# Kernel optimization log

Hardware: AMD Instinct MI355X
Metric: run time of the kernel (lower is better)

Reference implementation:

```python
import jax, jax.numpy as jnp
import numpy as np

EPS = 1e-5
NH = 8   # num_heads
P = 8    # patch_size (local window)

def layernorm(x, g, b):
    m = jnp.mean(x, axis=-1, keepdims=True)
    v = jnp.var(x, axis=-1, keepdims=True)
    return (x - m) * jax.lax.rsqrt(v + EPS) * g + b

def axis_embed(pos, nf):
    # DETR-style interleaved sin/cos along one axis -> (L, nf)
    dim_t = 10000.0 ** (2.0 * (jnp.arange(nf) // 2).astype(jnp.float32) / nf)
    p = pos[:, None] / dim_t
    return jnp.stack([jnp.sin(p[:, 0::2]), jnp.cos(p[:, 1::2])], axis=-1).reshape(pos.shape[0], nf)

def pos_embed_2d(E, H, W):
    # (H, W, E): first half of channels encode y, second half encode x
    half = E // 2
    ye = axis_embed(jnp.arange(1, H + 1, dtype=jnp.float32), half)
    xe = axis_embed(jnp.arange(1, W + 1, dtype=jnp.float32), half)
    return jnp.concatenate([jnp.broadcast_to(ye[:, None, :], (H, W, half)),
                            jnp.broadcast_to(xe[None, :, :], (H, W, half))], axis=-1)

def pos_embed_1d(L, E):
    # standard sinusoidal, (L, 1, E)
    pos = jnp.arange(L, dtype=jnp.float32)[:, None]
    div = jnp.exp(jnp.arange(0, E, 2, dtype=jnp.float32) * (-np.log(10000.0) / E))
    pe = jnp.zeros((L, E), jnp.float32)
    pe = pe.at[:, 0::2].set(jnp.sin(pos * div)).at[:, 1::2].set(jnp.cos(pos * div))
    return pe[:, None, :]

def mha(q, k, v, Wq, bq, Wk, bk, Wv, bv, Wo, bo, nh):
    # q,k,v: (B, L, C)
    B, Lq, C = q.shape
    hd = C // nh
    qh = (q @ Wq + bq).reshape(B, Lq, nh, hd)
    kh = (k @ Wk + bk).reshape(B, -1, nh, hd)
    vh = (v @ Wv + bv).reshape(B, -1, nh, hd)
    att = jax.nn.softmax(jnp.einsum('bqhd,bkhd->bhqk', qh, kh) / np.sqrt(hd).astype(np.float32), axis=-1)
    out = jnp.einsum('bhqk,bkhd->bqhd', att, vh).reshape(B, Lq, C)
    return out @ Wo + bo

def win_part(x):
    # (N,T,H,W,C) -> (N*T*nWin, P*P, C)
    N, T, H, W, C = x.shape
    x = x.reshape(N, T, H // P, P, W // P, P, C).transpose(0, 1, 2, 4, 3, 5, 6)
    return x.reshape(-1, P * P, C)

def forward(x, g1, b1, g2, b2, g3, b3, g4, b4,
            sWq, sbq, sWk, sbk, sWv, sbv, sWo, sbo,
            cW1, cb1, dwk, dwb, cW2, cb2,
            tWq, tbq, tWk, tbk, tWv, tbv, tWo, tbo,
            fW1, fb1, fW2, fb2):
    N, T, H, W, C = x.shape
    sl_pos = jnp.tile(pos_embed_2d(C, P, P), (H // P, W // P, 1))  # (H,W,C)
    tem_pos = pos_embed_1d(T, C)                                   # (T,1,C)

    # --- spatial local windowed MHSA (q=k=norm1(x+pos), v=norm1(x)) ---
    qk = win_part(layernorm(x + sl_pos, g1, b1))
    vv = win_part(layernorm(x, g1, b1))
    attn = mha(qk, qk, vv, sWq, sbq, sWk, sbk, sWv, sbv, sWo, sbo, NH)
    attn = attn.reshape(N, T, H // P, W // P, P, P, C).transpose(0, 1, 2, 4, 3, 5, 6).reshape(N, T, H, W, C)
    x = x + attn

    # --- Conv FFN: linear -> depthwise 3x3 -> GELU -> linear ---
    h = layernorm(x, g2, b2) @ cW1 + cb1
    Ch = h.shape[-1]
    h = h.reshape(N * T, H, W, Ch).transpose(0, 3, 1, 2)  # NCHW
    h = jax.lax.conv_general_dilated(h, dwk, (1, 1), 'SAME', feature_group_count=Ch,
                                     dimension_numbers=('NCHW', 'OIHW', 'NCHW')) + dwb[None, :, None, None]
    h = jax.nn.gelu(h, approximate=False)
    h = h.transpose(0, 2, 3, 1).reshape(N, T, H, W, Ch)
    x = x + (h @ cW2 + cb2)

    # --- temporal MHSA over T, tokens are (n,h,w) positions ---
    xt = x.transpose(1, 0, 2, 3, 4).reshape(T, N * H * W, C)
    xt = layernorm(xt, g3, b3)
    qt = layernorm(xt + tem_pos, g3, b3).transpose(1, 0, 2)  # (B,T,C)
    vt = layernorm(xt, g3, b3).transpose(1, 0, 2)
    xt = xt + mha(qt, qt, vt, tWq, tbq, tWk, tbk, tWv, tbv, tWo, tbo, NH).transpose(1, 0, 2)

    # --- FFN; original does x = x + drop3(x) (no residual, doubles output) ---
    xt = layernorm(xt, g4, b4)
    xt = jax.nn.gelu(xt @ fW1 + fb1, approximate=False) @ fW2 + fb2
    xt = xt + xt
    return xt.reshape(T, N, H, W, C).transpose(1, 0, 2, 3, 4)

def setup_inputs() -> dict:
    key = jax.random.key(0)
    N, T, H, W, C, DFF, HID = 4, 16, 32, 32, 256, 1024, 1024
    ks = iter(jax.random.split(key, 64))
    def w(*s):
        return jax.random.normal(next(ks), s, jnp.float32) * 0.02
    inp = dict(x=jax.random.normal(next(ks), (N, T, H, W, C), jnp.float32))
    for i in ('1', '2', '3', '4'):
        inp['g' + i] = jnp.ones((C,), jnp.float32)
        inp['b' + i] = jnp.zeros((C,), jnp.float32)
    for pfx in ('s', 't'):
        inp.update({pfx + 'Wq': w(C, C), pfx + 'bq': jnp.zeros((C,), jnp.float32),
                    pfx + 'Wk': w(C, C), pfx + 'bk': jnp.zeros((C,), jnp.float32),
                    pfx + 'Wv': w(C, C), pfx + 'bv': jnp.zeros((C,), jnp.float32),
                    pfx + 'Wo': w(C, C), pfx + 'bo': jnp.zeros((C,), jnp.float32)})
    inp.update(cW1=w(C, HID), cb1=jnp.zeros((HID,), jnp.float32),
               dwk=w(HID, 1, 3, 3), dwb=jnp.zeros((HID,), jnp.float32),
               cW2=w(HID, C), cb2=jnp.zeros((C,), jnp.float32))
    inp.update(fW1=w(C, DFF), fb1=jnp.zeros((DFF,), jnp.float32),
               fW2=w(DFF, C), fb2=jnp.zeros((C,), jnp.float32))
    return inp

def reference(x, g1, b1, g2, b2, g3, b3, g4, b4,
              sWq, sbq, sWk, sbk, sWv, sbv, sWo, sbo,
              cW1, cb1, dwk, dwb, cW2, cb2,
              tWq, tbq, tWk, tbk, tWv, tbv, tWo, tbo,
              fW1, fb1, fW2, fb2):
    return forward(x, g1, b1, g2, b2, g3, b3, g4, b4,
                   sWq, sbq, sWk, sbk, sWv, sbv, sWo, sbo,
                   cW1, cb1, dwk, dwb, cW2, cb2,
                   tWq, tbq, tWk, tbk, tWv, tbv, tWo, tbo,
                   fW1, fb1, fW2, fb2)
```

## Files before the change

kernel.cpp:

```cpp
#include <hip/hip_runtime.h>
#include <hip/hip_bf16.h>

typedef unsigned short u16;
typedef unsigned int u32;
typedef __attribute__((ext_vector_type(4))) float f32x4;
typedef __attribute__((ext_vector_type(8))) short s16x8;

static constexpr int Nn = 4, Tt = 16, Hh = 32, Ww = 32, Cc = 256;
static constexpr int Ltok = Nn * Tt * Hh * Ww;

__device__ __forceinline__ float bf2f(u16 v) {
  union { u32 u; float f; } t; t.u = ((u32)v) << 16; return t.f;
}
__device__ __forceinline__ u16 f2bf(float f) {
  union { u32 u; float f; } t; t.f = f;
  return (u16)((t.u + 0x7fffu + ((t.u >> 16) & 1u)) >> 16);
}
__device__ __forceinline__ ushort4 pack4(float a, float b, float c, float d) {
  ushort4 r; r.x = f2bf(a); r.y = f2bf(b); r.z = f2bf(c); r.w = f2bf(d); return r;
}
__device__ __forceinline__ float geluf(float x) {
  return 0.5f * x * (1.0f + erff(x * 0.70710678118654752f));
}
__device__ __forceinline__ float wsum(float v) {
#pragma unroll
  for (int o = 32; o > 0; o >>= 1) v += __shfl_xor(v, o, 64);
  return v;
}
__device__ __forceinline__ void ln_stats(float a0, float a1, float a2, float a3,
                                         float& m, float& inv) {
  float s  = wsum(a0 + a1 + a2 + a3);
  float s2 = wsum(a0 * a0 + a1 * a1 + a2 * a2 + a3 * a3);
  m = s * (1.0f / 256.0f);
  float v = s2 * (1.0f / 256.0f) - m * m;
  inv = rsqrtf(v + 1e-5f);
}
__device__ __forceinline__ void gload16(const u16* g, u16* l) {
  __builtin_amdgcn_global_load_lds(
      (const __attribute__((address_space(1))) void*)g,
      (__attribute__((address_space(3))) void*)l, 16, 0, 0);
}

__global__ __launch_bounds__(256) void k_pos(float* __restrict__ pe2d,
                                             float* __restrict__ pe1d,
                                             float* __restrict__ dwkT,
                                             float* __restrict__ zb,
                                             const float* __restrict__ dwk) {
  int idx = blockIdx.x * 256 + threadIdx.x;
  if (idx < 16384) {
    int y = idx >> 11, r = idx & 2047, x = r >> 8, c = r & 255;
    float pos; int cc;
    if (c < 128) { pos = (float)(y + 1); cc = c; }
    else         { pos = (float)(x + 1); cc = c - 128; }
    float e = (float)(cc & ~1) * (1.0f / 128.0f);
    float v = pos / powf(10000.0f, e);
    pe2d[idx] = (cc & 1) ? cosf(v) : sinf(v);
  } else if (idx < 20480) {
    int i = idx - 16384;
    int t = i >> 8, c = i & 255;
    float e = (float)(c & ~1) * (1.0f / 256.0f);
    float v = (float)t * powf(10000.0f, -e);
    pe1d[i] = (c & 1) ? cosf(v) : sinf(v);
  } else if (idx < 29696) {
    int i = idx - 20480;
    int c = i & 1023, tap = i >> 10;
    dwkT[tap * 1024 + c] = dwk[c * 9 + tap];
  } else if (idx < 30720) {
    zb[idx - 29696] = 0.0f;
  }
}

__global__ __launch_bounds__(256) void k_wprep(
    const float* __restrict__ s0, const float* __restrict__ s1,
    const float* __restrict__ s2, const float* __restrict__ s3,
    const float* __restrict__ s4, const float* __restrict__ s5,
    const float* __restrict__ s6, const float* __restrict__ s7,
    const float* __restrict__ cW1, const float* __restrict__ cW2,
    const float* __restrict__ fW1, const float* __restrict__ fW2,
    u16* __restrict__ WT) {
  __shared__ float Ls[32][33];
  int b = blockIdx.x;
  const float* src; u16* dst; int Kd, Nd, tb;
  if (b < 512) {
    int seg = b >> 6; tb = b & 63; Kd = 256; Nd = 256;
    const float* tab[8] = {s0, s1, s2, s3, s4, s5, s6, s7};
    src = tab[seg]; dst = WT + seg * 65536;
  } else if (b < 768)  { tb = b - 512;  Kd = 256;  Nd = 1024; src = cW1; dst = WT + 524288; }
  else if (b < 1024)   { tb = b - 768;  Kd = 1024; Nd = 256;  src = cW2; dst = WT + 786432; }
  else if (b < 1280)   { tb = b - 1024; Kd = 256;  Nd = 1024; src = fW1; dst = WT + 1048576; }
  else                 { tb = b - 1280; Kd = 1024; Nd = 256;  src = fW2; dst = WT + 1310720; }
  int nt = Nd >> 5;
  int tk = tb / nt, tn = tb % nt;
  int r = threadIdx.x >> 3, c0 = (threadIdx.x & 7) * 4;
  float4 v = *(const float4*)&src[(size_t)(tk * 32 + r) * Nd + tn * 32 + c0];
  Ls[r][c0] = v.x; Ls[r][c0 + 1] = v.y; Ls[r][c0 + 2] = v.z; Ls[r][c0 + 3] = v.w;
  __syncthreads();
  *(ushort4*)&dst[(size_t)(tn * 32 + r) * Kd + tk * 32 + c0] =
      pack4(Ls[c0][r], Ls[c0 + 1][r], Ls[c0 + 2][r], Ls[c0 + 3][r]);
}

__global__ __launch_bounds__(256) void k_ln1(const float* __restrict__ x,
                                             const float* __restrict__ g,
                                             const float* __restrict__ b,
                                             const float* __restrict__ pe2d,
                                             u16* __restrict__ qk,
                                             u16* __restrict__ vv) {
  int l = blockIdx.x * 4 + (threadIdx.x >> 6);
  int lane = threadIdx.x & 63, c0 = lane * 4;
  int idx = l & 1023, hh = idx >> 5, ww = idx & 31;
  float4 xv = *(const float4*)&x[(size_t)l * Cc + c0];
  float4 pv = *(const float4*)&pe2d[(((hh & 7) << 3) | (ww & 7)) * Cc + c0];
  float q0 = xv.x + pv.x, q1 = xv.y + pv.y, q2 = xv.z + pv.z, q3 = xv.w + pv.w;
  float mx, ix, mq, iq;
  ln_stats(xv.x, xv.y, xv.z, xv.w, mx, ix);
  ln_stats(q0, q1, q2, q3, mq, iq);
  float4 gv = *(const float4*)&g[c0];
  float4 bv = *(const float4*)&b[c0];
  *(ushort4*)&qk[(size_t)l * Cc + c0] =
      pack4((q0 - mq) * iq * gv.x + bv.x, (q1 - mq) * iq * gv.y + bv.y,
            (q2 - mq) * iq * gv.z + bv.z, (q3 - mq) * iq * gv.w + bv.w);
  *(ushort4*)&vv[(size_t)l * Cc + c0] =
      pack4((xv.x - mx) * ix * gv.x + bv.x, (xv.y - mx) * ix * gv.y + bv.y,
            (xv.z - mx) * ix * gv.z + bv.z, (xv.w - mx) * ix * gv.w + bv.w);
}

__global__ __launch_bounds__(256) void k_lnb(const u16* __restrict__ x,
                                             const float* __restrict__ g,
                                             const float* __restrict__ b,
                                             u16* __restrict__ out) {
  int l = blockIdx.x * 4 + (threadIdx.x >> 6);
  int lane = threadIdx.x & 63, c0 = lane * 4;
  ushort4 xv4 = *(const ushort4*)&x[(size_t)l * Cc + c0];
  float x0 = bf2f(xv4.x), x1 = bf2f(xv4.y), x2 = bf2f(xv4.z), x3 = bf2f(xv4.w);
  float m, inv;
  ln_stats(x0, x1, x2, x3, m, inv);
  float4 gv = *(const float4*)&g[c0];
  float4 bv = *(const float4*)&b[c0];
  *(ushort4*)&out[(size_t)l * Cc + c0] =
      pack4((x0 - m) * inv * gv.x + bv.x, (x1 - m) * inv * gv.y + bv.y,
            (x2 - m) * inv * gv.z + bv.z, (x3 - m) * inv * gv.w + bv.w);
}

__global__ __launch_bounds__(256) void k_ln3b(const u16* __restrict__ xa,
                                              const float* __restrict__ g,
                                              const float* __restrict__ b,
                                              const float* __restrict__ pe1d,
                                              u16* __restrict__ xt_base,
                                              u16* __restrict__ qt,
                                              u16* __restrict__ vt) {
  int l = blockIdx.x * 4 + (threadIdx.x >> 6);
  int lane = threadIdx.x & 63, c0 = lane * 4;
  ushort4 xv4 = *(const ushort4*)&xa[(size_t)l * Cc + c0];
  float x0 = bf2f(xv4.x), x1 = bf2f(xv4.y), x2 = bf2f(xv4.z), x3 = bf2f(xv4.w);
  float4 gv = *(const float4*)&g[c0];
  float4 bv = *(const float4*)&b[c0];
  float m, inv;
  ln_stats(x0, x1, x2, x3, m, inv);
  float t0 = (x0 - m) * inv * gv.x + bv.x;
  float t1 = (x1 - m) * inv * gv.y + bv.y;
  float t2 = (x2 - m) * inv * gv.z + bv.z;
  float t3 = (x3 - m) * inv * gv.w + bv.w;
  *(ushort4*)&xt_base[(size_t)l * Cc + c0] = pack4(t0, t1, t2, t3);
  float m2, inv2;
  ln_stats(t0, t1, t2, t3, m2, inv2);
  *(ushort4*)&vt[(size_t)l * Cc + c0] =
      pack4((t0 - m2) * inv2 * gv.x + bv.x, (t1 - m2) * inv2 * gv.y + bv.y,
            (t2 - m2) * inv2 * gv.z + bv.z, (t3 - m2) * inv2 * gv.w + bv.w);
  int tt = (l >> 10) & 15;
  float4 pv = *(const float4*)&pe1d[tt * Cc + c0];
  float s0 = t0 + pv.x, s1 = t1 + pv.y, s2 = t2 + pv.z, s3 = t3 + pv.w;
  float m3, inv3;
  ln_stats(s0, s1, s2, s3, m3, inv3);
  *(ushort4*)&qt[(size_t)l * Cc + c0] =
      pack4((s0 - m3) * inv3 * gv.x + bv.x, (s1 - m3) * inv3 * gv.y + bv.y,
            (s2 - m3) * inv3 * gv.z + bv.z, (s3 - m3) * inv3 * gv.w + bv.w);
}

template <int MODE>
__global__ __launch_bounds__(256, 2) void k_sgemm(const u16* __restrict__ A,
                                                  const u16* __restrict__ WT,
                                                  const float* __restrict__ bias,
                                                  const void* __restrict__ res,
                                                  void* __restrict__ out,
                                                  int ldout) {
  __shared__ u16 SMEM[32768];
  const int tid = threadIdx.x;
  const int wave = tid >> 6, lane = tid & 63;
  const int fr = lane & 15, fs = lane >> 4;
  const int r0base = blockIdx.x * 128;
  s16x8 wreg[4][8];
#pragma unroll
  for (int ni = 0; ni < 4; ++ni)
#pragma unroll
    for (int kt = 0; kt < 8; ++kt)
      wreg[ni][kt] = *(const s16x8*)&WT[(size_t)(wave * 64 + ni * 16 + fr) * 256 +
                                        kt * 32 + fs * 8];
  auto stage = [&](int buf, int r0) {
    u16* Ad = SMEM + buf * 8192;
#pragma unroll
    for (int i = 0; i < 4; ++i) {
      int idx = i * 256 + tid;
      int row = idx >> 5, s = idx & 31;
      gload16(A + (size_t)(r0 + row) * 256 + ((s ^ row) << 3), &Ad[idx * 8]);
    }
  };
  float* sc = (float*)(SMEM + 16384) + wave * 2048;
  stage(0, r0base);
  __syncthreads();
#pragma unroll 1
  for (int c = 0; c < 4; ++c) {
    if (c < 3) stage((c + 1) & 1, r0base + (c + 1) * 32);
    const u16* As = SMEM + (c & 1) * 8192;
    f32x4 acc[2][4] = {};
#pragma unroll
    for (int kt = 0; kt < 8; ++kt) {
      s16x8 a0 = *(const s16x8*)&As[(fr * 32 + ((kt * 4 + fs) ^ fr)) * 8];
      s16x8 a1 = *(const s16x8*)&As[((16 + fr) * 32 + ((kt * 4 + fs) ^ (16 + fr))) * 8];
#pragma unroll
      for (int ni = 0; ni < 4; ++ni) {
        acc[0][ni] = __builtin_amdgcn_mfma_f32_16x16x32_bf16(a0, wreg[ni][kt],
                                                             acc[0][ni], 0, 0, 0);
        acc[1][ni] = __builtin_amdgcn_mfma_f32_16x16x32_bf16(a1, wreg[ni][kt],
                                                             acc[1][ni], 0, 0, 0);
      }
    }
    const int r0 = r0base + c * 32;
    if constexpr (MODE == 5) {
      u16* o = (u16*)out;
#pragma unroll
      for (int ni = 0; ni < 4; ++ni) {
        int gc = wave * 64 + ni * 16 + fr;
        float bv = bias[gc];
#pragma unroll
        for (int mi = 0; mi < 2; ++mi) {
          int gr = r0 + mi * 16 + fs * 4;
          *(ushort4*)&o[(size_t)gc * (size_t)Ltok + gr] =
              pack4(acc[mi][ni][0] + bv, acc[mi][ni][1] + bv,
                    acc[mi][ni][2] + bv, acc[mi][ni][3] + bv);
        }
      }
    } else {
#pragma unroll
      for (int mi = 0; mi < 2; ++mi)
#pragma unroll
        for (int ni = 0; ni < 4; ++ni)
#pragma unroll
          for (int r = 0; r < 4; ++r) {
            int row = mi * 16 + fs * 4 + r;
            int col = ni * 16 + fr;
            sc[row * 64 + (col ^ ((row & 7) << 3))] = acc[mi][ni][r];
          }
#pragma unroll
      for (int p = 0; p < 8; ++p) {
        int row = p * 4 + (lane >> 4);
        int c4 = (lane & 15) * 4;
        f32x4 v4 = *(const f32x4*)&sc[row * 64 + (c4 ^ ((row & 7) << 3))];
        int gr = r0 + row;
        int gc = wave * 64 + c4;
        float4 bv4 = *(const float4*)&bias[gc];
        float v[4] = {v4[0] + bv4.x, v4[1] + bv4.y, v4[2] + bv4.z, v4[3] + bv4.w};
        size_t o = (size_t)gr * (size_t)ldout + gc;
        if constexpr (MODE == 1) {
#pragma unroll
          for (int j = 0; j < 4; ++j) v[j] = geluf(v[j]);
        }
        if constexpr (MODE == 3) {
          ushort4 r4 = *(const ushort4*)&((const u16*)res)[(size_t)gr * 256 + gc];
          v[0] += bf2f(r4.x); v[1] += bf2f(r4.y); v[2] += bf2f(r4.z); v[3] += bf2f(r4.w);
        }
        if constexpr (MODE == 7) {
          float4 r4 = *(const float4*)&((const float*)res)[(size_t)gr * 256 + gc];
          v[0] += r4.x; v[1] += r4.y; v[2] += r4.z; v[3] += r4.w;
        }
        *(ushort4*)&((u16*)out)[o] = pack4(v[0], v[1], v[2], v[3]);
      }
    }
    __syncthreads();
  }
}

template <int MODE>
__global__ __launch_bounds__(256) void k_mgemm(const u16* __restrict__ A,
                                               const u16* __restrict__ BT, int ldbt,
                                               const float* __restrict__ bias,
                                               const float* __restrict__ bias2,
                                               const void* __restrict__ res,
                                               void* __restrict__ out,
                                               int M, int N, int K) {
  __shared__ u16 SMEM[2 * 8192];
  const int tid = threadIdx.x;
  const int wave = tid >> 6, lane = tid & 63;
  const int m0 = blockIdx.x * 128, n0 = blockIdx.y * 128;
  const int wm = wave >> 1, wn = wave & 1;
  const int srow = tid >> 2;
  const int scol = (((tid & 3) ^ (srow & 3)) << 3);
  const u16* Ap = A + (size_t)(m0 + srow) * K + scol;
  const u16* Bp = BT + (size_t)(n0 + srow) * ldbt + scol;
  const int ldst = (wave * 64) * 8;
  const int fr = lane & 15, fs = lane >> 4;
  f32x4 acc[4][4] = {};
  auto stage = [&](int buf, int k0) {
    u16* Ad = SMEM + buf * 8192;
    u16* Bd = Ad + 4096;
#pragma unroll
    for (int it = 0; it < 2; ++it) {
      gload16(Ap + (size_t)(it * 64) * K + k0, &Ad[ldst + it * 2048]);
      gload16(Bp + (size_t)(it * 64) * ldbt + k0, &Bd[ldst + it * 2048]);
    }
  };
  auto compute = [&](int buf) {
    const u16* As = SMEM + buf * 8192;
    const u16* Bs = As + 4096;
    s16x8 af[4], bfr[4];
#pragma unroll
    for (int i = 0; i < 4; ++i) {
      int ra = wm * 64 + i * 16 + fr;
      af[i] = *(const s16x8*)&As[ra * 32 + ((fs ^ (ra & 3)) << 3)];
      int rb = wn * 64 + i * 16 + fr;
      bfr[i] = *(const s16x8*)&Bs[rb * 32 + ((fs ^ (rb & 3)) << 3)];
    }
#pragma unroll
    for (int mi = 0; mi < 4; ++mi)
#pragma unroll
      for (int ni = 0; ni < 4; ++ni)
        acc[mi][ni] = __builtin_amdgcn_mfma_f32_16x16x32_bf16(af[mi], bfr[ni],
                                                              acc[mi][ni], 0, 0, 0);
  };
  stage(0, 0);
  __syncthreads();
  const int nt = K >> 5;
  int cur = 0;
  for (int t = 0; t < nt - 1; ++t) {
    stage(cur ^ 1, (t + 1) << 5);
    compute(cur);
    __syncthreads();
    cur ^= 1;
  }
  compute(cur);
  __syncthreads();
  float* Wl = (float*)SMEM + wave * 2048;
#pragma unroll
  for (int nh = 0; nh < 2; ++nh) {
#pragma unroll
    for (int mi = 0; mi < 4; ++mi)
#pragma unroll
      for (int nq = 0; nq < 2; ++nq) {
        int ni = nh * 2 + nq;
#pragma unroll
        for (int r = 0; r < 4; ++r) {
          int row = mi * 16 + fs * 4 + r;
          int col = nq * 16 + fr;
          Wl[row * 32 + (col ^ ((row & 7) << 2))] = acc[mi][ni][r];
        }
      }
#pragma unroll
    for (int p = 0; p < 8; ++p) {
      int row = p * 8 + (lane >> 3);
      int c4 = (lane & 7) * 4;
      f32x4 v4 = *(const f32x4*)&Wl[row * 32 + (c4 ^ ((row & 7) << 2))];
      int gr = m0 + wm * 64 + row;
      int gc = n0 + wn * 64 + nh * 32 + c4;
      float4 bv4 = *(const float4*)&bias[gc];
      float v[4] = {v4[0] + bv4.x, v4[1] + bv4.y, v4[2] + bv4.z, v4[3] + bv4.w};
      const size_t o = (size_t)gr * (size_t)N + gc;
      if constexpr (MODE == 3) {
        ushort4 r4 = *(const ushort4*)&((const u16*)res)[o];
        v[0] += bf2f(r4.x); v[1] += bf2f(r4.y); v[2] += bf2f(r4.z); v[3] += bf2f(r4.w);
      }
      if constexpr (MODE == 4) {
#pragma unroll
        for (int j = 0; j < 4; ++j) v[j] *= 2.0f;
      }
      if constexpr (MODE == 4) {
        *(float4*)&((float*)out)[o] = make_float4(v[0], v[1], v[2], v[3]);
      } else {
        *(ushort4*)&((u16*)out)[o] = pack4(v[0], v[1], v[2], v[3]);
      }
    }
  }
}

__global__ __launch_bounds__(256) void k_sattn2(const u16* __restrict__ Q,
                                                const u16* __restrict__ Kb,
                                                const u16* __restrict__ VT,
                                                u16* __restrict__ ctx) {
  __shared__ u16 P_lds[4][4096];
  const int tid = threadIdx.x;
  const int wave = tid >> 6, lane = tid & 63;
  const int fr = lane & 15, fs = lane >> 4;
  const int wi = blockIdx.x >> 1;
  const int head = (blockIdx.x & 1) * 4 + wave;
  const int ft = wi >> 4, wy = (wi >> 2) & 3, wx = wi & 3;
  const int base = ft * 1024 + wy * 256 + wx * 8;
  const float scale = 0.17677669529663688f;
  const int ch = head * 32 + fs * 8;
  s16x8 ka[4], qb[4];
#pragma unroll
  for (int t4 = 0; t4 < 4; ++t4) {
    int tok = base + (2 * t4 + (fr >> 3)) * 32 + (fr & 7);
    ka[t4] = *(const s16x8*)&Kb[(size_t)tok * 256 + ch];
    qb[t4] = *(const s16x8*)&Q[(size_t)tok * 256 + ch];
  }
  f32x4 s[4][4] = {};
#pragma unroll
  for (int kt = 0; kt < 4; ++kt)
#pragma unroll
    for (int qt = 0; qt < 4; ++qt)
      s[kt][qt] = __builtin_amdgcn_mfma_f32_16x16x32_bf16(ka[kt], qb[qt], s[kt][qt], 0, 0, 0);
  u16* pw = P_lds[wave];
#pragma unroll
  for (int qt = 0; qt < 4; ++qt) {
    float m = -1e30f;
#pragma unroll
    for (int kt = 0; kt < 4; ++kt)
#pragma unroll
      for (int r = 0; r < 4; ++r) m = fmaxf(m, s[kt][qt][r]);
    m = fmaxf(m, __shfl_xor(m, 16, 64));
    m = fmaxf(m, __shfl_xor(m, 32, 64));
    m *= scale;
    float e[4][4];
    float sum = 0.f;
#pragma unroll
    for (int kt = 0; kt < 4; ++kt)
#pragma unroll
      for (int r = 0; r < 4; ++r) {
        e[kt][r] = __expf(s[kt][qt][r] * scale - m);
        sum += e[kt][r];
      }
    sum += __shfl_xor(sum, 16, 64);
    sum += __shfl_xor(sum, 32, 64);
    float il = 1.0f / sum;
    int q = qt * 16 + fr;
    int rowb = q * 128, sw = (q & 7) << 4;
#pragma unroll
    for (int kt = 0; kt < 4; ++kt)
      *(ushort4*)((char*)pw + ((rowb + kt * 32 + fs * 8) ^ sw)) =
          pack4(e[kt][0] * il, e[kt][1] * il, e[kt][2] * il, e[kt][3] * il);
  }
  f32x4 o[4][2] = {};
#pragma unroll
  for (int ks = 0; ks < 2; ++ks) {
    s16x8 vb[2];
#pragma unroll
    for (int nt = 0; nt < 2; ++nt) {
      int d = head * 32 + nt * 16 + fr;
      int tok = base + (ks * 4 + fs) * 32;
      vb[nt] = *(const s16x8*)&VT[(size_t)d * (size_t)Ltok + tok];
    }
#pragma unroll
    for (int qt = 0; qt < 4; ++qt) {
      int q = qt * 16 + fr;
      s16x8 pa = *(const s16x8*)((char*)pw +
                                 ((q * 128 + ks * 64 + fs * 16) ^ ((q & 7) << 4)));
#pragma unroll
      for (int nt = 0; nt < 2; ++nt)
        o[qt][nt] = __builtin_amdgcn_mfma_f32_16x16x32_bf16(pa, vb[nt], o[qt][nt], 0, 0, 0);
    }
  }
#pragma unroll
  for (int qt = 0; qt < 4; ++qt)
#pragma unroll
    for (int r = 0; r < 4; ++r) {
      int q = qt * 16 + fs * 4 + r;
      int tok = base + (q >> 3) * 32 + (q & 7);
#pragma unroll
      for (int nt = 0; nt < 2; ++nt)
        ctx[(size_t)tok * 256 + head * 32 + nt * 16 + fr] = f2bf(o[qt][nt][r]);
    }
}

__global__ __launch_bounds__(256) void k_tattn2(const u16* __restrict__ Q,
                                                const u16* __restrict__ Kb,
                                                const u16* __restrict__ V,
                                                u16* __restrict__ ctx) {
  __shared__ u16 Vs[16 * 256];
  const int tid = threadIdx.x;
  const int b = blockIdx.x;
  const int n = b >> 10, hw = b & 1023;
  const int tok0 = n * 16384 + hw;
#pragma unroll
  for (int i = 0; i < 2; ++i) {
    int chunk = tid * 2 + i;
    int row = chunk >> 5, c8 = (chunk & 31) * 8;
    *(uint4*)&Vs[row * 256 + c8] =
        *(const uint4*)&V[(size_t)(tok0 + row * 1024) * 256 + c8];
  }
  __syncthreads();
  const int wave = tid >> 6, lane = tid & 63;
  const int fr = lane & 15, fs = lane >> 4;
  const float scale = 0.17677669529663688f;
#pragma unroll
  for (int hg = 0; hg < 2; ++hg) {
    int head = wave + hg * 4;
    int ch = head * 32 + fs * 8;
    size_t go = (size_t)(tok0 + fr * 1024) * 256 + ch;
    s16x8 ka = *(const s16x8*)&Kb[go];
    s16x8 qb = *(const s16x8*)&Q[go];
    f32x4 s = {0.f, 0.f, 0.f, 0.f};
    s = __builtin_amdgcn_mfma_f32_16x16x32_bf16(ka, qb, s, 0, 0, 0);
    float m = fmaxf(fmaxf(s[0], s[1]), fmaxf(s[2], s[3]));
    m = fmaxf(m, __shfl_xor(m, 16, 64));
    m = fmaxf(m, __shfl_xor(m, 32, 64));
    m *= scale;
    float e0 = __expf(s[0] * scale - m), e1 = __expf(s[1] * scale - m);
    float e2 = __expf(s[2] * scale - m), e3 = __expf(s[3] * scale - m);
    float sum = e0 + e1 + e2 + e3;
    sum += __shfl_xor(sum, 16, 64);
    sum += __shfl_xor(sum, 32, 64);
    float il = 1.0f / sum;
    e0 *= il; e1 *= il; e2 *= il; e3 *= il;
    float o[8] = {};
#pragma unroll
    for (int kb = 0; kb < 4; ++kb) {
      int src = kb * 16 + fr;
      float p0 = __shfl(e0, src, 64);
      float p1 = __shfl(e1, src, 64);
      float p2 = __shfl(e2, src, 64);
      float p3 = __shfl(e3, src, 64);
#pragma unroll
      for (int r = 0; r < 4; ++r) {
        float p = r == 0 ? p0 : (r == 1 ? p1 : (r == 2 ? p2 : p3));
        uint4 vv = *(const uint4*)&Vs[(kb * 4 + r) * 256 + ch];
        const u16* vp = (const u16*)&vv;
#pragma unroll
        for (int u = 0; u < 8; ++u) o[u] = fmaf(p, bf2f(vp[u]), o[u]);
      }
    }
    size_t co = (size_t)(tok0 + fr * 1024) * 256 + ch;
    *(ushort4*)&ctx[co] = pack4(o[0], o[1], o[2], o[3]);
    *(ushort4*)&ctx[co + 4] = pack4(o[4], o[5], o[6], o[7]);
  }
}

__global__ __launch_bounds__(256) void k_dwconv(const u16* __restrict__ Hin,
                                                const float* __restrict__ dwkT,
                                                const float* __restrict__ dwb,
                                                int ch0, int oco,
                                                u16* __restrict__ Hout) {
  int flat = blockIdx.x * 256 + threadIdx.x;
  int l = flat >> 5, cg = flat & 31, c0 = cg * 8, tc0 = ch0 + c0;
  int frame = l >> 10, idx = l & 1023, hh = idx >> 5, ww = idx & 31;
  float acc[8];
  *(float4*)&acc[0] = *(const float4*)&dwb[tc0];
  *(float4*)&acc[4] = *(const float4*)&dwb[tc0 + 4];
#pragma unroll
  for (int ky = -1; ky <= 1; ++ky) {
    int h2 = hh + ky;
    if (h2 < 0 || h2 >= 32) continue;
#pragma unroll
    for (int kx = -1; kx <= 1; ++kx) {
      int w2 = ww + kx;
      if (w2 < 0 || w2 >= 32) continue;
      int ln = frame * 1024 + h2 * 32 + w2;
      uint4 hv = *(const uint4*)&Hin[(size_t)ln * 256 + c0];
      const u16* hp = (const u16*)&hv;
      int tap = (ky + 1) * 3 + (kx + 1);
      float wk[8];
      *(float4*)&wk[0] = *(const float4*)&dwkT[tap * 1024 + tc0];
      *(float4*)&wk[4] = *(const float4*)&dwkT[tap * 1024 + tc0 + 4];
#pragma unroll
      for (int u = 0; u < 8; ++u) acc[u] = fmaf(bf2f(hp[u]), wk[u], acc[u]);
    }
  }
  size_t ob = (size_t)l * 512 + oco + c0;
  *(ushort4*)&Hout[ob] = pack4(geluf(acc[0]), geluf(acc[1]), geluf(acc[2]), geluf(acc[3]));
  *(ushort4*)&Hout[ob + 4] = pack4(geluf(acc[4]), geluf(acc[5]), geluf(acc[6]), geluf(acc[7]));
}

extern "C" void kernel_launch(void* const* d_in, const int* in_sizes, int n_in,
                              void* d_out, int out_size, void* d_ws, size_t ws_size,
                              hipStream_t stream) {
  (void)in_sizes; (void)n_in; (void)out_size; (void)ws_size;
  const float* x   = (const float*)d_in[0];
  const float* g1  = (const float*)d_in[1];  const float* b1  = (const float*)d_in[2];
  const float* g2  = (const float*)d_in[3];  const float* b2  = (const float*)d_in[4];
  const float* g3  = (const float*)d_in[5];  const float* b3  = (const float*)d_in[6];
  const float* g4  = (const float*)d_in[7];  const float* b4  = (const float*)d_in[8];
  const float* sWq = (const float*)d_in[9];  const float* sbq = (const float*)d_in[10];
  const float* sWk = (const float*)d_in[11]; const float* sbk = (const float*)d_in[12];
  const float* sWv = (const float*)d_in[13]; const float* sbv = (const float*)d_in[14];
  const float* sWo = (const float*)d_in[15]; const float* sbo = (const float*)d_in[16];
  const float* tWq = (const float*)d_in[17]; const float* tbq = (const float*)d_in[18];
  const float* tWk = (const float*)d_in[19]; const float* tbk = (const float*)d_in[20];
  const float* tWv = (const float*)d_in[21]; const float* tbv = (const float*)d_in[22];
  const float* tWo = (const float*)d_in[23]; const float* tbo = (const float*)d_in[24];
  const float* cW1 = (const float*)d_in[25]; const float* cb1 = (const float*)d_in[26];
  const float* dwk = (const float*)d_in[27]; const float* dwb = (const float*)d_in[28];
  const float* cW2 = (const float*)d_in[29]; const float* cb2 = (const float*)d_in[30];
  const float* fW1 = (const float*)d_in[31]; const float* fb1 = (const float*)d_in[32];
  const float* fW2 = (const float*)d_in[33]; const float* fb2 = (const float*)d_in[34];

  char* ws = (char*)d_ws;
  const size_t MB = 1ull << 20;
  float* PE2D = (float*)(ws);
  float* PE1D = (float*)(ws + (64 << 10));
  float* DWKT = (float*)(ws + (80 << 10));
  float* ZB   = (float*)(ws + (116 << 10));
  u16*   WT   = (u16*)(ws + (128 << 10));
  u16* XA = (u16*)(ws + 4 * MB);
  u16* X1 = (u16*)(ws + 4 * MB);
  u16* B1 = (u16*)(ws + 68 * MB);
  u16* B2 = (u16*)(ws + 100 * MB);
  u16* B3 = (u16*)(ws + 132 * MB);
  u16* B4 = (u16*)(ws + 164 * MB);
  u16* F1 = (u16*)(ws + 4 * MB);
  u16* H1q = B2;
  u16* H2h = B3;

  u16* sWqT = WT;               u16* sWkT = WT + 65536;
  u16* sWvT = WT + 2 * 65536;   u16* sWoT = WT + 3 * 65536;
  u16* tWqT = WT + 4 * 65536;   u16* tWkT = WT + 5 * 65536;
  u16* tWvT = WT + 6 * 65536;   u16* tWoT = WT + 7 * 65536;
  u16* cW1T = WT + 524288;      u16* cW2T = WT + 786432;
  u16* fW1T = WT + 1048576;     u16* fW2T = WT + 1310720;

  dim3 blk(256);
  dim3 gLN(Ltok / 4);
  dim3 gS(512);
  dim3 g2d(Ltok / 128, 2);

  k_pos<<<dim3(120), blk, 0, stream>>>(PE2D, PE1D, DWKT, ZB, dwk);
  k_wprep<<<dim3(1536), blk, 0, stream>>>(sWq, sWk, sWv, sWo, tWq, tWk, tWv, tWo,
                                          cW1, cW2, fW1, fW2, WT);
  k_ln1<<<gLN, blk, 0, stream>>>(x, g1, b1, PE2D, B1, B2);
  k_sgemm<5><<<gS, blk, 0, stream>>>(B2, sWvT, sbv, nullptr, B3, 0);
  k_sgemm<0><<<gS, blk, 0, stream>>>(B1, sWqT, sbq, nullptr, B2, 256);
  k_sgemm<0><<<gS, blk, 0, stream>>>(B1, sWkT, sbk, nullptr, B4, 256);
  k_sattn2<<<dim3(2048), blk, 0, stream>>>(B2, B4, B3, B1);
  k_sgemm<7><<<gS, blk, 0, stream>>>(B1, sWoT, sbo, x, XA, 256);
  k_lnb<<<gLN, blk, 0, stream>>>(XA, g2, b2, B1);
  for (int h = 0; h < 2; ++h) {
    for (int qq = 0; qq < 2; ++qq) {
      int q = h * 2 + qq;
      k_sgemm<0><<<gS, blk, 0, stream>>>(B1, cW1T + q * 65536, cb1 + q * 256,
                                         nullptr, H1q, 256);
      k_dwconv<<<dim3(Ltok * 32 / 256), blk, 0, stream>>>(H1q, DWKT, dwb,
                                                          q * 256, qq * 256, H2h);
    }
    k_mgemm<3><<<g2d, blk, 0, stream>>>(H2h, cW2T + h * 512, 1024,
                                        h ? cb2 : ZB, nullptr, XA, XA,
                                        Ltok, 256, 512);
  }
  k_ln3b<<<gLN, blk, 0, stream>>>(XA, g3, b3, PE1D, B1, B2, B3);
  k_sgemm<0><<<gS, blk, 0, stream>>>(B3, tWvT, tbv, nullptr, B4, 256);
  k_sgemm<0><<<gS, blk, 0, stream>>>(B2, tWqT, tbq, nullptr, X1, 256);
  k_sgemm<0><<<gS, blk, 0, stream>>>(B2, tWkT, tbk, nullptr, B3, 256);
  k_tattn2<<<dim3(4096), blk, 0, stream>>>(X1, B3, B4, B2);
  k_sgemm<3><<<gS, blk, 0, stream>>>(B2, tWoT, tbo, B1, B3, 256);
  k_lnb<<<gLN, blk, 0, stream>>>(B3, g4, b4, B4);
  for (int q = 0; q < 4; ++q)
    k_sgemm<1><<<gS, blk, 0, stream>>>(B4, fW1T + q * 65536, fb1 + q * 256,
                                       nullptr, F1 + q * 256, 1024);
  k_mgemm<4><<<g2d, blk, 0, stream>>>(F1, fW2T, 1024, fb2, nullptr, nullptr,
                                      (float*)d_out, Ltok, 256, 1024);
}
```

Before: 785.5 us.

## Batch weight-slab GEMMs via 2D grid and replace mgemm with register-weight GEMMs

Merges separate per-slab projection launches (Q/K, conv expansion halves, FFN up quarters) into single 2D-grid launches of the register-resident-weight GEMM, using concatenated biases prepared in the setup kernel. The generic tiled k_mgemm for the K=512 and K=1024 down-projections is replaced by specialized kernels that keep weight columns in registers and stream A rows through LDS. The sgemm epilogue now applies bias and GELU before staging bf16 instead of fp32, which shrinks LDS. This cuts launch count and re-reads, but the new kernels hold many weight registers, which may hurt occupancy, and they rely on new buffer aliasing.

```diff
diff --git a/kernel.cpp b/kernel.cpp
--- a/kernel.cpp
+++ b/kernel.cpp
@@ -45,7 +45,13 @@
                                              float* __restrict__ pe1d,
                                              float* __restrict__ dwkT,
                                              float* __restrict__ zb,
-                                             const float* __restrict__ dwk) {
+                                             float* __restrict__ sqk,
+                                             float* __restrict__ tqk,
+                                             const float* __restrict__ dwk,
+                                             const float* __restrict__ sbq,
+                                             const float* __restrict__ sbk,
+                                             const float* __restrict__ tbq,
+                                             const float* __restrict__ tbk) {
   int idx = blockIdx.x * 256 + threadIdx.x;
   if (idx < 16384) {
     int y = idx >> 11, r = idx & 2047, x = r >> 8, c = r & 255;
@@ -67,6 +73,12 @@
     dwkT[tap * 1024 + c] = dwk[c * 9 + tap];
   } else if (idx < 30720) {
     zb[idx - 29696] = 0.0f;
+  } else if (idx < 31232) {
+    int i = idx - 30720;
+    sqk[i] = (i < 256) ? sbq[i] : sbk[i - 256];
+  } else if (idx < 31744) {
+    int i = idx - 31232;
+    tqk[i] = (i < 256) ? tbq[i] : tbk[i - 256];
   }
 }
 
@@ -179,15 +191,21 @@
 template <int MODE>
 __global__ __launch_bounds__(256, 2) void k_sgemm(const u16* __restrict__ A,
                                                   const u16* __restrict__ WT,
+                                                  int wt_stride,
                                                   const float* __restrict__ bias,
+                                                  int bias_stride,
                                                   const void* __restrict__ res,
                                                   void* __restrict__ out,
-                                                  int ldout) {
-  __shared__ u16 SMEM[32768];
+                                                  size_t out_xoff, int ldout) {
+  __shared__ u16 SMEM[24576];
   const int tid = threadIdx.x;
   const int wave = tid >> 6, lane = tid & 63;
   const int fr = lane & 15, fs = lane >> 4;
-  const int r0base = blockIdx.x * 128;
+  const int bx = blockIdx.x;
+  const int r0base = blockIdx.y * 128;
+  WT += (size_t)bx * wt_stride;
+  bias += bx * bias_stride;
+  u16* ob = (u16*)out + (size_t)bx * out_xoff;
   s16x8 wreg[4][8];
 #pragma unroll
   for (int ni = 0; ni < 4; ++ni)
@@ -204,7 +222,7 @@
       gload16(A + (size_t)(r0 + row) * 256 + ((s ^ row) << 3), &Ad[idx * 8]);
     }
   };
-  float* sc = (float*)(SMEM + 16384) + wave * 2048;
+  u16* sc = SMEM + 16384 + wave * 2048;
   stage(0, r0base);
   __syncthreads();
 #pragma unroll 1
@@ -241,142 +259,179 @@
       }
     } else {
 #pragma unroll
-      for (int mi = 0; mi < 2; ++mi)
-#pragma unroll
-        for (int ni = 0; ni < 4; ++ni)
+      for (int ni = 0; ni < 4; ++ni) {
+        float bv = bias[wave * 64 + ni * 16 + fr];
+#pragma unroll
+        for (int mi = 0; mi < 2; ++mi)
 #pragma unroll
           for (int r = 0; r < 4; ++r) {
             int row = mi * 16 + fs * 4 + r;
             int col = ni * 16 + fr;
-            sc[row * 64 + (col ^ ((row & 7) << 3))] = acc[mi][ni][r];
+            float v = acc[mi][ni][r] + bv;
+            if constexpr (MODE == 1) v = geluf(v);
+            sc[row * 64 + (col ^ ((row & 3) << 3))] = f2bf(v);
           }
-#pragma unroll
-      for (int p = 0; p < 8; ++p) {
-        int row = p * 4 + (lane >> 4);
-        int c4 = (lane & 15) * 4;
-        f32x4 v4 = *(const f32x4*)&sc[row * 64 + (c4 ^ ((row & 7) << 3))];
+      }
+#pragma unroll
+      for (int p = 0; p < 4; ++p) {
+        int row = p * 8 + (lane >> 3);
+        int c8 = (lane & 7) * 8;
+        ushort4 u0 = *(const ushort4*)&sc[row * 64 + ((c8 ^ ((row & 3) << 3)))];
+        ushort4 u1 = *(const ushort4*)&sc[row * 64 + (((c8 + 4) ^ ((row & 3) << 3)))];
         int gr = r0 + row;
-        int gc = wave * 64 + c4;
-        float4 bv4 = *(const float4*)&bias[gc];
-        float v[4] = {v4[0] + bv4.x, v4[1] + bv4.y, v4[2] + bv4.z, v4[3] + bv4.w};
+        int gc = wave * 64 + c8;
         size_t o = (size_t)gr * (size_t)ldout + gc;
-        if constexpr (MODE == 1) {
-#pragma unroll
-          for (int j = 0; j < 4; ++j) v[j] = geluf(v[j]);
-        }
         if constexpr (MODE == 3) {
-          ushort4 r4 = *(const ushort4*)&((const u16*)res)[(size_t)gr * 256 + gc];
-          v[0] += bf2f(r4.x); v[1] += bf2f(r4.y); v[2] += bf2f(r4.z); v[3] += bf2f(r4.w);
+          const u16* rp = (const u16*)res;
+          ushort4 r0v = *(const ushort4*)&rp[(size_t)gr * 256 + gc];
+          ushort4 r1v = *(const ushort4*)&rp[(size_t)gr * 256 + gc + 4];
+          u0 = pack4(bf2f(u0.x) + bf2f(r0v.x), bf2f(u0.y) + bf2f(r0v.y),
+                     bf2f(u0.z) + bf2f(r0v.z), bf2f(u0.w) + bf2f(r0v.w));
+          u1 = pack4(bf2f(u1.x) + bf2f(r1v.x), bf2f(u1.y) + bf2f(r1v.y),
+                     bf2f(u1.z) + bf2f(r1v.z), bf2f(u1.w) + bf2f(r1v.w));
         }
         if constexpr (MODE == 7) {
-          float4 r4 = *(const float4*)&((const float*)res)[(size_t)gr * 256 + gc];
-          v[0] += r4.x; v[1] += r4.y; v[2] += r4.z; v[3] += r4.w;
+          const float* rp = (const float*)res;
+          float4 r0v = *(const float4*)&rp[(size_t)gr * 256 + gc];
+          float4 r1v = *(const float4*)&rp[(size_t)gr * 256 + gc + 4];
+          u0 = pack4(bf2f(u0.x) + r0v.x, bf2f(u0.y) + r0v.y,
+                     bf2f(u0.z) + r0v.z, bf2f(u0.w) + r0v.w);
+          u1 = pack4(bf2f(u1.x) + r1v.x, bf2f(u1.y) + r1v.y,
+                     bf2f(u1.z) + r1v.z, bf2f(u1.w) + r1v.w);
         }
-        *(ushort4*)&((u16*)out)[o] = pack4(v[0], v[1], v[2], v[3]);
+        *(ushort4*)&ob[o] = u0;
+        *(ushort4*)&ob[o + 4] = u1;
       }
     }
     __syncthreads();
   }
 }
 
-template <int MODE>
-__global__ __launch_bounds__(256) void k_mgemm(const u16* __restrict__ A,
-                                               const u16* __restrict__ BT, int ldbt,
-                                               const float* __restrict__ bias,
-                                               const float* __restrict__ bias2,
-                                               const void* __restrict__ res,
-                                               void* __restrict__ out,
-                                               int M, int N, int K) {
-  __shared__ u16 SMEM[2 * 8192];
+__global__ __launch_bounds__(256, 2) void k_cgemm(const u16* __restrict__ A,
+                                                  const u16* __restrict__ WT,
+                                                  const float* __restrict__ bias,
+                                                  u16* __restrict__ xa) {
+  __shared__ u16 SMEM[18432];
   const int tid = threadIdx.x;
   const int wave = tid >> 6, lane = tid & 63;
-  const int m0 = blockIdx.x * 128, n0 = blockIdx.y * 128;
-  const int wm = wave >> 1, wn = wave & 1;
-  const int srow = tid >> 2;
-  const int scol = (((tid & 3) ^ (srow & 3)) << 3);
-  const u16* Ap = A + (size_t)(m0 + srow) * K + scol;
-  const u16* Bp = BT + (size_t)(n0 + srow) * ldbt + scol;
-  const int ldst = (wave * 64) * 8;
   const int fr = lane & 15, fs = lane >> 4;
-  f32x4 acc[4][4] = {};
-  auto stage = [&](int buf, int k0) {
+  const int bx = blockIdx.x;
+  const int r0base = blockIdx.y * 128;
+  s16x8 wreg[2][16];
+#pragma unroll
+  for (int ni = 0; ni < 2; ++ni)
+#pragma unroll
+    for (int kt = 0; kt < 16; ++kt)
+      wreg[ni][kt] = *(const s16x8*)&WT[(size_t)(bx * 128 + wave * 32 + ni * 16 + fr) *
+                                            1024 + kt * 32 + fs * 8];
+  auto stage = [&](int buf, int r0) {
     u16* Ad = SMEM + buf * 8192;
-    u16* Bd = Ad + 4096;
-#pragma unroll
-    for (int it = 0; it < 2; ++it) {
-      gload16(Ap + (size_t)(it * 64) * K + k0, &Ad[ldst + it * 2048]);
-      gload16(Bp + (size_t)(it * 64) * ldbt + k0, &Bd[ldst + it * 2048]);
+#pragma unroll
+    for (int i = 0; i < 4; ++i) {
+      int idx = i * 256 + tid;
+      int row = idx >> 6, s = idx & 63;
+      gload16(A + (size_t)(r0 + row) * 512 + ((s ^ (row & 7)) << 3), &Ad[idx * 8]);
     }
   };
-  auto compute = [&](int buf) {
-    const u16* As = SMEM + buf * 8192;
-    const u16* Bs = As + 4096;
-    s16x8 af[4], bfr[4];
-#pragma unroll
-    for (int i = 0; i < 4; ++i) {
-      int ra = wm * 64 + i * 16 + fr;
-      af[i] = *(const s16x8*)&As[ra * 32 + ((fs ^ (ra & 3)) << 3)];
-      int rb = wn * 64 + i * 16 + fr;
-      bfr[i] = *(const s16x8*)&Bs[rb * 32 + ((fs ^ (rb & 3)) << 3)];
-    }
-#pragma unroll
-    for (int mi = 0; mi < 4; ++mi)
-#pragma unroll
-      for (int ni = 0; ni < 4; ++ni)
-        acc[mi][ni] = __builtin_amdgcn_mfma_f32_16x16x32_bf16(af[mi], bfr[ni],
-                                                              acc[mi][ni], 0, 0, 0);
+  u16* sc = SMEM + 16384 + wave * 512;
+  stage(0, r0base);
+  __syncthreads();
+#pragma unroll 1
+  for (int c = 0; c < 8; ++c) {
+    if (c < 7) stage((c + 1) & 1, r0base + (c + 1) * 16);
+    const u16* As = SMEM + (c & 1) * 8192;
+    f32x4 acc[2] = {};
+#pragma unroll
+    for (int kt = 0; kt < 16; ++kt) {
+      s16x8 a = *(const s16x8*)&As[fr * 512 + (((kt * 4 + fs) ^ (fr & 7)) << 3)];
+#pragma unroll
+      for (int ni = 0; ni < 2; ++ni)
+        acc[ni] = __builtin_amdgcn_mfma_f32_16x16x32_bf16(a, wreg[ni][kt],
+                                                          acc[ni], 0, 0, 0);
+    }
+    const int r0 = r0base + c * 16;
+#pragma unroll
+    for (int ni = 0; ni < 2; ++ni) {
+      float bv = bias[bx * 128 + wave * 32 + ni * 16 + fr];
+#pragma unroll
+      for (int r = 0; r < 4; ++r) {
+        int row = fs * 4 + r;
+        int col = ni * 16 + fr;
+        sc[row * 32 + (col ^ ((row & 3) << 3))] = f2bf(acc[ni][r] + bv);
+      }
+    }
+    {
+      int row = lane >> 2, c8 = (lane & 3) * 8;
+      ushort4 u0 = *(const ushort4*)&sc[row * 32 + (c8 ^ ((row & 3) << 3))];
+      ushort4 u1 = *(const ushort4*)&sc[row * 32 + ((c8 + 4) ^ ((row & 3) << 3))];
+      int gr = r0 + row;
+      int gc = bx * 128 + wave * 32 + c8;
+      size_t o = (size_t)gr * 256 + gc;
+      ushort4 r0v = *(const ushort4*)&xa[o];
+      ushort4 r1v = *(const ushort4*)&xa[o + 4];
+      *(ushort4*)&xa[o] = pack4(bf2f(u0.x) + bf2f(r0v.x), bf2f(u0.y) + bf2f(r0v.y),
+                                bf2f(u0.z) + bf2f(r0v.z), bf2f(u0.w) + bf2f(r0v.w));
+      *(ushort4*)&xa[o + 4] = pack4(bf2f(u1.x) + bf2f(r1v.x), bf2f(u1.y) + bf2f(r1v.y),
+                                    bf2f(u1.z) + bf2f(r1v.z), bf2f(u1.w) + bf2f(r1v.w));
+    }
+    __syncthreads();
+  }
+}
+
+__global__ __launch_bounds__(256, 2) void k_fgemm(const u16* __restrict__ A,
+                                                  const u16* __restrict__ WT,
+                                                  const float* __restrict__ bias,
+                                                  float* __restrict__ out) {
+  __shared__ u16 SMEM[34816];
+  const int tid = threadIdx.x;
+  const int wave = tid >> 6, lane = tid & 63;
+  const int fr = lane & 15, fs = lane >> 4;
+  const int bx = blockIdx.x;
+  const int r0base = blockIdx.y * 128;
+  const int col = bx * 64 + wave * 16 + fr;
+  s16x8 wreg[32];
+#pragma unroll
+  for (int kt = 0; kt < 32; ++kt)
+    wreg[kt] = *(const s16x8*)&WT[(size_t)col * 1024 + kt * 32 + fs * 8];
+  auto stage = [&](int buf, int r0) {
+    u16* Ad = SMEM + buf * 16384;
+#pragma unroll
+    for (int i = 0; i < 8; ++i) {
+      int idx = i * 256 + tid;
+      int row = idx >> 7, s = idx & 127;
+      gload16(A + (size_t)(r0 + row) * 1024 + ((s ^ (row & 7)) << 3), &Ad[idx * 8]);
+    }
   };
-  stage(0, 0);
+  float* scf = (float*)(SMEM + 32768) + wave * 256;
+  stage(0, r0base);
   __syncthreads();
-  const int nt = K >> 5;
-  int cur = 0;
-  for (int t = 0; t < nt - 1; ++t) {
-    stage(cur ^ 1, (t + 1) << 5);
-    compute(cur);
+#pragma unroll 1
+  for (int c = 0; c < 8; ++c) {
+    if (c < 7) stage((c + 1) & 1, r0base + (c + 1) * 16);
+    const u16* As = SMEM + (c & 1) * 16384;
+    f32x4 acc = {};
+#pragma unroll
+    for (int kt = 0; kt < 32; ++kt) {
+      s16x8 a = *(const s16x8*)&As[fr * 1024 + (((kt * 4 + fs) ^ (fr & 7)) << 3)];
+      acc = __builtin_amdgcn_mfma_f32_16x16x32_bf16(a, wreg[kt], acc, 0, 0, 0);
+    }
+    const int r0 = r0base + c * 16;
+    {
+      float bv = bias[col];
+#pragma unroll
+      for (int r = 0; r < 4; ++r) {
+        int row = fs * 4 + r;
+        scf[row * 16 + (fr ^ ((row & 3) << 2))] = 2.0f * (acc[r] + bv);
+      }
+    }
+    {
+      int row = lane >> 2, c4 = (lane & 3) * 4;
+      f32x4 v4 = *(const f32x4*)&scf[row * 16 + (c4 ^ ((row & 3) << 2))];
+      int gr = r0 + row;
+      *(float4*)&out[(size_t)gr * 256 + bx * 64 + wave * 16 + c4] =
+          make_float4(v4[0], v4[1], v4[2], v4[3]);
+    }
     __syncthreads();
-    cur ^= 1;
-  }
-  compute(cur);
-  __syncthreads();
-  float* Wl = (float*)SMEM + wave * 2048;
-#pragma unroll
-  for (int nh = 0; nh < 2; ++nh) {
-#pragma unroll
-    for (int mi = 0; mi < 4; ++mi)
-#pragma unroll
-      for (int nq = 0; nq < 2; ++nq) {
-        int ni = nh * 2 + nq;
-#pragma unroll
-        for (int r = 0; r < 4; ++r) {
-          int row = mi * 16 + fs * 4 + r;
-          int col = nq * 16 + fr;
-          Wl[row * 32 + (col ^ ((row & 7) << 2))] = acc[mi][ni][r];
-        }
-      }
-#pragma unroll
-    for (int p = 0; p < 8; ++p) {
-      int row = p * 8 + (lane >> 3);
-      int c4 = (lane & 7) * 4;
-      f32x4 v4 = *(const f32x4*)&Wl[row * 32 + (c4 ^ ((row & 7) << 2))];
-      int gr = m0 + wm * 64 + row;
-      int gc = n0 + wn * 64 + nh * 32 + c4;
-      float4 bv4 = *(const float4*)&bias[gc];
-      float v[4] = {v4[0] + bv4.x, v4[1] + bv4.y, v4[2] + bv4.z, v4[3] + bv4.w};
-      const size_t o = (size_t)gr * (size_t)N + gc;
-      if constexpr (MODE == 3) {
-        ushort4 r4 = *(const ushort4*)&((const u16*)res)[o];
-        v[0] += bf2f(r4.x); v[1] += bf2f(r4.y); v[2] += bf2f(r4.z); v[3] += bf2f(r4.w);
-      }
-      if constexpr (MODE == 4) {
-#pragma unroll
-        for (int j = 0; j < 4; ++j) v[j] *= 2.0f;
-      }
-      if constexpr (MODE == 4) {
-        *(float4*)&((float*)out)[o] = make_float4(v[0], v[1], v[2], v[3]);
-      } else {
-        *(ushort4*)&((u16*)out)[o] = pack4(v[0], v[1], v[2], v[3]);
-      }
-    }
   }
 }
 
@@ -596,61 +651,64 @@
   float* PE1D = (float*)(ws + (64 << 10));
   float* DWKT = (float*)(ws + (80 << 10));
   float* ZB   = (float*)(ws + (116 << 10));
+  float* SQK  = (float*)(ws + (120 << 10));
+  float* TQK  = (float*)(ws + (122 << 10));
   u16*   WT   = (u16*)(ws + (128 << 10));
-  u16* XA = (u16*)(ws + 4 * MB);
-  u16* X1 = (u16*)(ws + 4 * MB);
-  u16* B1 = (u16*)(ws + 68 * MB);
-  u16* B2 = (u16*)(ws + 100 * MB);
-  u16* B3 = (u16*)(ws + 132 * MB);
-  u16* B4 = (u16*)(ws + 164 * MB);
-  u16* F1 = (u16*)(ws + 4 * MB);
-  u16* H1q = B2;
-  u16* H2h = B3;
-
-  u16* sWqT = WT;               u16* sWkT = WT + 65536;
+  u16* XA  = (u16*)(ws + 4 * MB);
+  u16* X1  = (u16*)(ws + 4 * MB);
+  u16* H1A = (u16*)(ws + 36 * MB);
+  u16* B1  = (u16*)(ws + 68 * MB);
+  u16* B2  = (u16*)(ws + 100 * MB);
+  u16* B3  = (u16*)(ws + 132 * MB);
+  u16* B4  = (u16*)(ws + 164 * MB);
+  u16* H1B = B4;
+  u16* H2h = B2;
+  u16* F1  = (u16*)(ws + 4 * MB);
+
+  u16* sWqT = WT;
   u16* sWvT = WT + 2 * 65536;   u16* sWoT = WT + 3 * 65536;
-  u16* tWqT = WT + 4 * 65536;   u16* tWkT = WT + 5 * 65536;
+  u16* tWqT = WT + 4 * 65536;
   u16* tWvT = WT + 6 * 65536;   u16* tWoT = WT + 7 * 65536;
   u16* cW1T = WT + 524288;      u16* cW2T = WT + 786432;
   u16* fW1T = WT + 1048576;     u16* fW2T = WT + 1310720;
 
   dim3 blk(256);
   dim3 gLN(Ltok / 4);
-  dim3 gS(512);
-  dim3 g2d(Ltok / 128, 2);
-
-  k_pos<<<dim3(120), blk, 0, stream>>>(PE2D, PE1D, DWKT, ZB, dwk);
+
+  k_pos<<<dim3(124), blk, 0, stream>>>(PE2D, PE1D, DWKT, ZB, SQK, TQK,
+                                       dwk, sbq, sbk, tbq, tbk);
   k_wprep<<<dim3(1536), blk, 0, stream>>>(sWq, sWk, sWv, sWo, tWq, tWk, tWv, tWo,
                                           cW1, cW2, fW1, fW2, WT);
   k_ln1<<<gLN, blk, 0, stream>>>(x, g1, b1, PE2D, B1, B2);
-  k_sgemm<5><<<gS, blk, 0, stream>>>(B2, sWvT, sbv, nullptr, B3, 0);
-  k_sgemm<0><<<gS, blk, 0, stream>>>(B1, sWqT, sbq, nullptr, B2, 256);
-  k_sgemm<0><<<gS, blk, 0, stream>>>(B1, sWkT, sbk, nullptr, B4, 256);
+  k_sgemm<5><<<dim3(1, 512), blk, 0, stream>>>(B2, sWvT, 0, sbv, 0, nullptr,
+                                               B3, 0, 0);
+  k_sgemm<0><<<dim3(2, 512), blk, 0, stream>>>(B1, sWqT, 65536, SQK, 256, nullptr,
+                                               B2, 33554432ull, 256);
   k_sattn2<<<dim3(2048), blk, 0, stream>>>(B2, B4, B3, B1);
-  k_sgemm<7><<<gS, blk, 0, stream>>>(B1, sWoT, sbo, x, XA, 256);
+  k_sgemm<7><<<dim3(1, 512), blk, 0, stream>>>(B1, sWoT, 0, sbo, 0, x,
+                                               XA, 0, 256);
   k_lnb<<<gLN, blk, 0, stream>>>(XA, g2, b2, B1);
   for (int h = 0; h < 2; ++h) {
-    for (int qq = 0; qq < 2; ++qq) {
-      int q = h * 2 + qq;
-      k_sgemm<0><<<gS, blk, 0, stream>>>(B1, cW1T + q * 65536, cb1 + q * 256,
-                                         nullptr, H1q, 256);
-      k_dwconv<<<dim3(Ltok * 32 / 256), blk, 0, stream>>>(H1q, DWKT, dwb,
-                                                          q * 256, qq * 256, H2h);
-    }
-    k_mgemm<3><<<g2d, blk, 0, stream>>>(H2h, cW2T + h * 512, 1024,
-                                        h ? cb2 : ZB, nullptr, XA, XA,
-                                        Ltok, 256, 512);
+    k_sgemm<0><<<dim3(2, 512), blk, 0, stream>>>(B1, cW1T + h * 2 * 65536, 65536,
+                                                 cb1 + h * 512, 256, nullptr,
+                                                 H1A, 67108864ull, 256);
+    k_dwconv<<<dim3(Ltok * 32 / 256), blk, 0, stream>>>(H1A, DWKT, dwb,
+                                                        (h * 2) * 256, 0, H2h);
+    k_dwconv<<<dim3(Ltok * 32 / 256), blk, 0, stream>>>(H1B, DWKT, dwb,
+                                                        (h * 2 + 1) * 256, 256, H2h);
+    k_cgemm<<<dim3(2, 512), blk, 0, stream>>>(H2h, cW2T + h * 512,
+                                              h ? cb2 : ZB, XA);
   }
   k_ln3b<<<gLN, blk, 0, stream>>>(XA, g3, b3, PE1D, B1, B2, B3);
-  k_sgemm<0><<<gS, blk, 0, stream>>>(B3, tWvT, tbv, nullptr, B4, 256);
-  k_sgemm<0><<<gS, blk, 0, stream>>>(B2, tWqT, tbq, nullptr, X1, 256);
-  k_sgemm<0><<<gS, blk, 0, stream>>>(B2, tWkT, tbk, nullptr, B3, 256);
+  k_sgemm<0><<<dim3(1, 512), blk, 0, stream>>>(B3, tWvT, 0, tbv, 0, nullptr,
+                                               B4, 0, 256);
+  k_sgemm<0><<<dim3(2, 512), blk, 0, stream>>>(B2, tWqT, 65536, TQK, 256, nullptr,
+                                               X1, 67108864ull, 256);
   k_tattn2<<<dim3(4096), blk, 0, stream>>>(X1, B3, B4, B2);
-  k_sgemm<3><<<gS, blk, 0, stream>>>(B2, tWoT, tbo, B1, B3, 256);
+  k_sgemm<3><<<dim3(1, 512), blk, 0, stream>>>(B2, tWoT, 0, tbo, 0, B1,
+                                               B3, 0, 256);
   k_lnb<<<gLN, blk, 0, stream>>>(B3, g4, b4, B4);
-  for (int q = 0; q < 4; ++q)
-    k_sgemm<1><<<gS, blk, 0, stream>>>(B4, fW1T + q * 65536, fb1 + q * 256,
-                                       nullptr, F1 + q * 256, 1024);
-  k_mgemm<4><<<g2d, blk, 0, stream>>>(F1, fW2T, 1024, fb2, nullptr, nullptr,
-                                      (float*)d_out, Ltok, 256, 1024);
-}
+  k_sgemm<1><<<dim3(4, 512), blk, 0, stream>>>(B4, fW1T, 65536, fb1, 256, nullptr,
+                                               F1, 256ull, 1024);
+  k_fgemm<<<dim3(4, 512), blk, 0, stream>>>(F1, fW2T, fb2, (float*)d_out);
+}
```

Result: no change. 794.6 us (+1.2%).
